# Kernel optimization log

Hardware: AMD Instinct MI355X
Metric: run time of the kernel (lower is better)

## Reference

```python
import jax, jax.numpy as jnp
import numpy as np


def make_dictionary(T, Drr, Dtheta):
    # rows i=0..T-1; (-Drr)**i == (-1)**i * Drr**i for integer i
    idx = jnp.arange(T, dtype=Drr.dtype)[:, None]                      # [T,1]
    sign = jnp.where(jnp.arange(T)[:, None] % 2 == 0, 1.0, -1.0).astype(Drr.dtype)
    ri = Drr[None, :] ** idx                                           # [T,N]
    c = jnp.cos(idx * Dtheta[None, :])
    s = jnp.sin(idx * Dtheta[None, :])
    dic = jnp.concatenate(
        [jnp.ones((T, 1), Drr.dtype), ri * c, sign * ri * c, ri * s, sign * ri * s],
        axis=1,
    )                                                                  # [T, 1+4N]
    G = jnp.linalg.norm(dic, axis=0)
    G = jnp.where(G == 0, jnp.sqrt(jnp.asarray(T, dic.dtype)), G)
    return dic / G


def softshrink(x, lam):
    return jnp.sign(x) * jnp.maximum(jnp.abs(x) - lam, 0.0)


def fista(D, Y, lambd=0.1, max_iter=100, tol=1e-4):
    # D: [T,K], Y: [B,T,F]
    K = D.shape[1]
    DtD = D.T @ D                                                      # [K,K]
    linv = 1.0 / jnp.linalg.norm(DtD)  # torch.norm(DtD, 2) == Frobenius norm
    DtY = jnp.einsum('tk,btf->bkf', D, Y) * linv                       # [B,K,F]
    A = jnp.eye(K, dtype=D.dtype) - DtD * linv
    lam = lambd * linv
    x0 = jnp.zeros_like(DtY)

    def cond(s):
        _, _, _, it, done = s
        return (it < max_iter) & jnp.logical_not(done)

    def body(s):
        x_old, y_old, t, it, done = s
        x_new = softshrink(jnp.einsum('kj,bjf->bkf', A, y_old) + DtY, lam)
        t_new = (1.0 + jnp.sqrt(1.0 + 4.0 * t * t)) / 2.0
        tt = (t - 1.0) / t_new
        y_new = (1.0 + tt) * x_new - tt * x_old
        conv = jnp.linalg.norm((x_new - x_old).ravel()) / K < tol
        return (x_new, y_new, jnp.where(conv, t, t_new), it + 1, conv)

    s0 = (x0, x0, jnp.asarray(1.0, D.dtype), jnp.asarray(0, jnp.int32),
          jnp.asarray(False))
    x, _, _, _, _ = jax.lax.while_loop(cond, body, s0)
    return x


def setup_inputs() -> dict:
    key = jax.random.key(0)
    k1, k2, k3 = jax.random.split(key, 3)
    return {
        'x': jax.random.normal(k1, (2, 36, 20480), jnp.float32),
        'Drr': jax.random.uniform(k2, (40,), dtype=jnp.float32),
        'Dtheta': jax.random.uniform(k3, (40,), dtype=jnp.float32),
        'T': 36,
    }


def reference(x, Drr, Dtheta, T):
    D = make_dictionary(T, Drr, Dtheta)
    return fista(D, x, lambd=0.1, max_iter=100)
```

## Files before the change

### kernel.cpp

```cpp
#include <hip/hip_runtime.h>
#include <math.h>

typedef _Float16 half8 __attribute__((ext_vector_type(8)));
typedef _Float16 half4 __attribute__((ext_vector_type(4)));
typedef float    f32x4 __attribute__((ext_vector_type(4)));

#define T_DIM 36
#define N_AT 40
#define K_REAL 161
#define MT 12
#define KS 6
#define KS2 2
#define B_DIM 2
#define F_DIM 20480
#define CB 16
#define MLOC 3
#define NTHREADS 256
#define SETUP_T 512
#define MAXIT 100
#define YK 200
#define YST 72

#define WS_AFRAG_OFF 64
#define AFRAG_BYTES (144 * 1024)
#define WS_DFRAG_OFF (WS_AFRAG_OFF + AFRAG_BYTES)

#define MFMA16(a, b, c) __builtin_amdgcn_mfma_f32_16x16x32_f16((a), (b), (c), 0, 0, 0)

__global__ void setup_kernel(const float* __restrict__ Drr,
                             const float* __restrict__ Dtheta,
                             float* __restrict__ ws) {
    __shared__ float Dl[K_REAL][T_DIM];
    __shared__ float red[SETUP_T];
    __shared__ float s_linv;
    int tid = threadIdx.x;

    if (tid < K_REAL) {
        float col[T_DIM];
        if (tid == 0) {
            for (int i = 0; i < T_DIM; ++i) col[i] = 1.0f;
        } else {
            int q = (tid - 1) / N_AT, n = (tid - 1) % N_AT;
            float r = Drr[n], th = Dtheta[n];
            float ri = 1.0f;
            for (int i = 0; i < T_DIM; ++i) {
                float c = cosf((float)i * th), s = sinf((float)i * th);
                float sign = (i & 1) ? -1.0f : 1.0f;
                float v;
                if (q == 0)      v = ri * c;
                else if (q == 1) v = sign * ri * c;
                else if (q == 2) v = ri * s;
                else             v = sign * ri * s;
                col[i] = v;
                ri *= r;
            }
        }
        float ss = 0.0f;
        for (int i = 0; i < T_DIM; ++i) ss += col[i] * col[i];
        float G = sqrtf(ss);
        float Ginv = (G == 0.0f) ? (1.0f / sqrtf((float)T_DIM)) : (1.0f / G);
        for (int i = 0; i < T_DIM; ++i) Dl[tid][i] = col[i] * Ginv;
    }
    __syncthreads();

    float local = 0.0f;
    for (int p = tid; p < K_REAL * K_REAL; p += SETUP_T) {
        int a = p / K_REAL, b = p % K_REAL;
        float dot = 0.0f;
        for (int i = 0; i < T_DIM; ++i) dot += Dl[a][i] * Dl[b][i];
        local += dot * dot;
    }
    red[tid] = local;
    __syncthreads();
    if (tid == 0) {
        float tot = 0.0f;
        for (int i = 0; i < SETUP_T; ++i) tot += red[i];
        float linv = 1.0f / sqrtf(tot);
        s_linv = linv;
        ws[0] = linv;
        ws[1] = 0.1f * linv;
    }
    __syncthreads();
    float linv = s_linv;

    _Float16* wsA = (_Float16*)((char*)ws + WS_AFRAG_OFF);
    int lane = tid >> 3, e = tid & 7;
    int fm = lane & 15, fq = lane >> 4;
    for (int p = 0; p < MT * KS; ++p) {
        int Mt = p / KS, ks = p % KS;
        int m = Mt * 16 + fm;
        int k = ks * 32 + fq * 8 + e;
        float v = 0.0f;
        if (m < K_REAL && k < K_REAL) {
            float dot = 0.0f;
            for (int t = 0; t < T_DIM; ++t) dot += Dl[m][t] * Dl[k][t];
            v = ((m == k) ? 1.0f : 0.0f) - linv * dot;
        }
        _Float16 h = (_Float16)v;
        _Float16 l = (_Float16)(v - (float)h);
        int base = (p * 2) * 512 + lane * 8 + e;
        wsA[base]       = h;
        wsA[base + 512] = l;
    }

    _Float16* wsD = (_Float16*)((char*)ws + WS_DFRAG_OFF);
    for (int p = 0; p < MT * KS2; ++p) {
        int Mt = p / KS2, ks2 = p % KS2;
        int kr = Mt * 16 + fm;
        int t  = ks2 * 32 + fq * 8 + e;
        float v = (kr < K_REAL && t < T_DIM) ? linv * Dl[kr][t] : 0.0f;
        _Float16 h = (_Float16)v;
        _Float16 l = (_Float16)(v - (float)h);
        int base = (p * 2) * 512 + lane * 8 + e;
        wsD[base]       = h;
        wsD[base + 512] = l;
    }
}

__global__ void __launch_bounds__(NTHREADS, 2)
fista_mfma(const float* __restrict__ Y, const float* __restrict__ ws,
           float* __restrict__ out) {
    __shared__ __align__(16) _Float16 ybuf[2][2][CB][YK];

    const float lam = ((const float*)ws)[1];
    const half8* Afp = (const half8*)((const char*)ws + WS_AFRAG_OFF);
    const half8* Dfp = (const half8*)((const char*)ws + WS_DFRAG_OFF);

    const int tid  = threadIdx.x;
    const int lane = tid & 63;
    const int mg   = __builtin_amdgcn_readfirstlane(tid >> 6);
    const int quad = lane >> 4;
    const int cl   = lane & 15;

    const int blk = blockIdx.x;
    const int b   = blk / (F_DIM / CB);
    const int f0  = (blk % (F_DIM / CB)) * CB;

    _Float16* Yst = &ybuf[1][0][0][0];
    const float* Yb = Y + (size_t)b * T_DIM * F_DIM + f0;
    for (int idx = tid; idx < 64 * CB; idx += NTHREADS) {
        int t = idx / CB, c = idx % CB;
        float v = (t < T_DIM) ? Yb[(size_t)t * F_DIM + c] : 0.0f;
        _Float16 h = (_Float16)v;
        _Float16 l = (_Float16)(v - (float)h);
        Yst[c * YST + t]            = h;
        Yst[CB * YST + c * YST + t] = l;
    }
    int4* zb = (int4*)&ybuf[0][0][0][0];
    for (int idx = tid; idx < (2 * CB * YK * 2) / 16; idx += NTHREADS)
        zb[idx] = int4{0, 0, 0, 0};
    __syncthreads();

    f32x4 dty[MLOC];
    #pragma unroll
    for (int ml = 0; ml < MLOC; ++ml) dty[ml] = f32x4{0.f, 0.f, 0.f, 0.f};
    #pragma unroll
    for (int ks2 = 0; ks2 < KS2; ++ks2) {
        const _Float16* yp = Yst + cl * YST + ks2 * 32 + quad * 8;
        half8 yh = *(const half8*)yp;
        half8 yl = *(const half8*)(yp + CB * YST);
        #pragma unroll
        for (int ml = 0; ml < MLOC; ++ml) {
            int Mt = mg * MLOC + ml;
            half8 dh = Dfp[((Mt * KS2 + ks2) * 2 + 0) * 64 + lane];
            half8 dl = Dfp[((Mt * KS2 + ks2) * 2 + 1) * 64 + lane];
            dty[ml] = MFMA16(dh, yh, dty[ml]);
            dty[ml] = MFMA16(dh, yl, dty[ml]);
            dty[ml] = MFMA16(dl, yh, dty[ml]);
        }
    }
    __syncthreads();

    half8 Af[MLOC][KS][2];
    #pragma unroll
    for (int ml = 0; ml < MLOC; ++ml)
        #pragma unroll
        for (int ks = 0; ks < KS; ++ks)
            #pragma unroll
            for (int term = 0; term < 2; ++term)
                Af[ml][ks][term] =
                    Afp[(((mg * MLOC + ml) * KS + ks) * 2 + term) * 64 + lane];

    float xold[MLOC][4];
    #pragma unroll
    for (int ml = 0; ml < MLOC; ++ml)
        #pragma unroll
        for (int r = 0; r < 4; ++r) xold[ml][r] = 0.0f;

    float tm = 1.0f;
    int p = 0;
    for (int it = 0; it < MAXIT; ++it) {
        f32x4 acc[MLOC];
        #pragma unroll
        for (int ml = 0; ml < MLOC; ++ml) acc[ml] = dty[ml];

        #pragma unroll
        for (int ks = 0; ks < KS; ++ks) {
            const _Float16* yp = &ybuf[p][0][cl][ks * 32 + quad * 8];
            half8 yh = *(const half8*)yp;
            half8 yl = *(const half8*)(yp + CB * YK);
            #pragma unroll
            for (int ml = 0; ml < MLOC; ++ml) {
                acc[ml] = MFMA16(Af[ml][ks][0], yh, acc[ml]);
                acc[ml] = MFMA16(Af[ml][ks][0], yl, acc[ml]);
                acc[ml] = MFMA16(Af[ml][ks][1], yh, acc[ml]);
            }
        }

        float tn = 0.5f * (1.0f + sqrtf(1.0f + 4.0f * tm * tm));
        float tt = (tm - 1.0f) / tn;
        tm = tn;

        #pragma unroll
        for (int ml = 0; ml < MLOC; ++ml) {
            half4 hv, lv;
            #pragma unroll
            for (int r = 0; r < 4; ++r) {
                float v  = acc[ml][r];
                float s  = fmaxf(fabsf(v) - lam, 0.0f);
                float xn = copysignf(s, v);
                float yn = (1.0f + tt) * xn - tt * xold[ml][r];
                xold[ml][r] = xn;
                _Float16 h = (_Float16)yn;
                hv[r] = h;
                lv[r] = (_Float16)(yn - (float)h);
            }
            int k0 = (mg * MLOC + ml) * 16 + quad * 4;
            *(half4*)&ybuf[1 - p][0][cl][k0] = hv;
            *(half4*)&ybuf[1 - p][1][cl][k0] = lv;
        }
        __syncthreads();
        p ^= 1;
    }

    float* ob = out + (size_t)b * K_REAL * F_DIM + f0 + cl;
    #pragma unroll
    for (int ml = 0; ml < MLOC; ++ml)
        #pragma unroll
        for (int r = 0; r < 4; ++r) {
            int k = (mg * MLOC + ml) * 16 + quad * 4 + r;
            if (k < K_REAL) ob[(size_t)k * F_DIM] = xold[ml][r];
        }
}

extern "C" void kernel_launch(void* const* d_in, const int* in_sizes, int n_in,
                              void* d_out, int out_size, void* d_ws, size_t ws_size,
                              hipStream_t stream) {
    const float* x      = (const float*)d_in[0];
    const float* Drr    = (const float*)d_in[1];
    const float* Dtheta = (const float*)d_in[2];
    float* out = (float*)d_out;
    float* ws  = (float*)d_ws;

    hipLaunchKernelGGL(setup_kernel, dim3(1), dim3(SETUP_T), 0, stream,
                       Drr, Dtheta, ws);
    hipLaunchKernelGGL(fista_mfma, dim3((B_DIM * F_DIM) / CB), dim3(NTHREADS),
                       0, stream, x, ws, out);
}
```

Measured before the change: 689.1 us.

## Switch FISTA iteration to 32x32x16 MFMA tiles with 32-column blocks

Replaces the 16x16x32 MFMA tiling with 32x32x16 MFMA. Each of six waves now owns a 32-row slice of the 192-padded coefficient dimension, and each block covers 32 F-columns instead of 16. The aim is to cut padding waste on the K dimension (from 192 to 176) and to halve the block count, so each A-fragment load and barrier serves more columns. The cost is larger per-wave accumulators and a changed occupancy target, and the last wave only partly fills its rows.

```diff
diff --git a/kernel.cpp b/kernel.cpp
--- a/kernel.cpp
+++ b/kernel.cpp
@@ -1,31 +1,32 @@
 #include <hip/hip_runtime.h>
 #include <math.h>
 
-typedef _Float16 half8 __attribute__((ext_vector_type(8)));
-typedef _Float16 half4 __attribute__((ext_vector_type(4)));
-typedef float    f32x4 __attribute__((ext_vector_type(4)));
+typedef _Float16 half8  __attribute__((ext_vector_type(8)));
+typedef _Float16 half4  __attribute__((ext_vector_type(4)));
+typedef float    f32x16 __attribute__((ext_vector_type(16)));
 
 #define T_DIM 36
 #define N_AT 40
 #define K_REAL 161
-#define MT 12
-#define KS 6
-#define KS2 2
+#define MT32 6
+#define KS16 11
+#define KT 3
 #define B_DIM 2
 #define F_DIM 20480
-#define CB 16
-#define MLOC 3
-#define NTHREADS 256
+#define CB 32
+#define NW 6
+#define NTHREADS (NW * 64)
 #define SETUP_T 512
 #define MAXIT 100
-#define YK 200
-#define YST 72
+#define YKH 200
+#define YSTH 104
 
 #define WS_AFRAG_OFF 64
-#define AFRAG_BYTES (144 * 1024)
+#define AFRAG_BYTES (MT32 * KS16 * 2 * 1024)
 #define WS_DFRAG_OFF (WS_AFRAG_OFF + AFRAG_BYTES)
-
-#define MFMA16(a, b, c) __builtin_amdgcn_mfma_f32_16x16x32_f16((a), (b), (c), 0, 0, 0)
+#define DFRAG_BYTES (MT32 * KT * 2 * 1024)
+
+#define MFMA32(a, b, c) __builtin_amdgcn_mfma_f32_32x32x16_f16((a), (b), (c), 0, 0, 0)
 
 __global__ void setup_kernel(const float* __restrict__ Drr,
                              const float* __restrict__ Dtheta,
@@ -85,11 +86,11 @@
 
     _Float16* wsA = (_Float16*)((char*)ws + WS_AFRAG_OFF);
     int lane = tid >> 3, e = tid & 7;
-    int fm = lane & 15, fq = lane >> 4;
-    for (int p = 0; p < MT * KS; ++p) {
-        int Mt = p / KS, ks = p % KS;
-        int m = Mt * 16 + fm;
-        int k = ks * 32 + fq * 8 + e;
+    int fm = lane & 31, fg = lane >> 5;
+    for (int p = 0; p < MT32 * KS16; ++p) {
+        int Mt = p / KS16, ks = p % KS16;
+        int m = Mt * 32 + fm;
+        int k = ks * 16 + fg * 8 + e;
         float v = 0.0f;
         if (m < K_REAL && k < K_REAL) {
             float dot = 0.0f;
@@ -104,10 +105,10 @@
     }
 
     _Float16* wsD = (_Float16*)((char*)ws + WS_DFRAG_OFF);
-    for (int p = 0; p < MT * KS2; ++p) {
-        int Mt = p / KS2, ks2 = p % KS2;
-        int kr = Mt * 16 + fm;
-        int t  = ks2 * 32 + fq * 8 + e;
+    for (int p = 0; p < MT32 * KT; ++p) {
+        int Mt = p / KT, ks2 = p % KT;
+        int kr = Mt * 32 + fm;
+        int t  = ks2 * 16 + fg * 8 + e;
         float v = (kr < K_REAL && t < T_DIM) ? linv * Dl[kr][t] : 0.0f;
         _Float16 h = (_Float16)v;
         _Float16 l = (_Float16)(v - (float)h);
@@ -117,10 +118,10 @@
     }
 }
 
-__global__ void __launch_bounds__(NTHREADS, 2)
+__global__ void __launch_bounds__(NTHREADS, 3)
 fista_mfma(const float* __restrict__ Y, const float* __restrict__ ws,
            float* __restrict__ out) {
-    __shared__ __align__(16) _Float16 ybuf[2][2][CB][YK];
+    __shared__ __align__(16) _Float16 ybuf[2][2][CB][YKH];
 
     const float lam = ((const float*)ws)[1];
     const half8* Afp = (const half8*)((const char*)ws + WS_AFRAG_OFF);
@@ -129,8 +130,8 @@
     const int tid  = threadIdx.x;
     const int lane = tid & 63;
     const int mg   = __builtin_amdgcn_readfirstlane(tid >> 6);
-    const int quad = lane >> 4;
-    const int cl   = lane & 15;
+    const int col  = lane & 31;
+    const int kg   = lane >> 5;
 
     const int blk = blockIdx.x;
     const int b   = blk / (F_DIM / CB);
@@ -138,73 +139,59 @@
 
     _Float16* Yst = &ybuf[1][0][0][0];
     const float* Yb = Y + (size_t)b * T_DIM * F_DIM + f0;
-    for (int idx = tid; idx < 64 * CB; idx += NTHREADS) {
-        int t = idx / CB, c = idx % CB;
+    for (int idx = tid; idx < 48 * CB; idx += NTHREADS) {
+        int t = idx >> 5, c = idx & 31;
         float v = (t < T_DIM) ? Yb[(size_t)t * F_DIM + c] : 0.0f;
         _Float16 h = (_Float16)v;
         _Float16 l = (_Float16)(v - (float)h);
-        Yst[c * YST + t]            = h;
-        Yst[CB * YST + c * YST + t] = l;
+        Yst[c * YSTH + t]             = h;
+        Yst[CB * YSTH + c * YSTH + t] = l;
     }
     int4* zb = (int4*)&ybuf[0][0][0][0];
-    for (int idx = tid; idx < (2 * CB * YK * 2) / 16; idx += NTHREADS)
+    for (int idx = tid; idx < (2 * CB * YKH * 2) / 16; idx += NTHREADS)
         zb[idx] = int4{0, 0, 0, 0};
     __syncthreads();
 
-    f32x4 dty[MLOC];
-    #pragma unroll
-    for (int ml = 0; ml < MLOC; ++ml) dty[ml] = f32x4{0.f, 0.f, 0.f, 0.f};
-    #pragma unroll
-    for (int ks2 = 0; ks2 < KS2; ++ks2) {
-        const _Float16* yp = Yst + cl * YST + ks2 * 32 + quad * 8;
+    f32x16 dty;
+    #pragma unroll
+    for (int r = 0; r < 16; ++r) dty[r] = 0.0f;
+    #pragma unroll
+    for (int ks2 = 0; ks2 < KT; ++ks2) {
+        const _Float16* yp = Yst + col * YSTH + ks2 * 16 + kg * 8;
         half8 yh = *(const half8*)yp;
-        half8 yl = *(const half8*)(yp + CB * YST);
+        half8 yl = *(const half8*)(yp + CB * YSTH);
+        half8 dh = Dfp[((mg * KT + ks2) * 2 + 0) * 64 + lane];
+        half8 dl = Dfp[((mg * KT + ks2) * 2 + 1) * 64 + lane];
+        dty = MFMA32(dh, yh, dty);
+        dty = MFMA32(dh, yl, dty);
+        dty = MFMA32(dl, yh, dty);
+    }
+    __syncthreads();
+
+    half8 Af[KS16][2];
+    #pragma unroll
+    for (int ks = 0; ks < KS16; ++ks)
         #pragma unroll
-        for (int ml = 0; ml < MLOC; ++ml) {
-            int Mt = mg * MLOC + ml;
-            half8 dh = Dfp[((Mt * KS2 + ks2) * 2 + 0) * 64 + lane];
-            half8 dl = Dfp[((Mt * KS2 + ks2) * 2 + 1) * 64 + lane];
-            dty[ml] = MFMA16(dh, yh, dty[ml]);
-            dty[ml] = MFMA16(dh, yl, dty[ml]);
-            dty[ml] = MFMA16(dl, yh, dty[ml]);
-        }
-    }
-    __syncthreads();
-
-    half8 Af[MLOC][KS][2];
-    #pragma unroll
-    for (int ml = 0; ml < MLOC; ++ml)
-        #pragma unroll
-        for (int ks = 0; ks < KS; ++ks)
-            #pragma unroll
-            for (int term = 0; term < 2; ++term)
-                Af[ml][ks][term] =
-                    Afp[(((mg * MLOC + ml) * KS + ks) * 2 + term) * 64 + lane];
-
-    float xold[MLOC][4];
-    #pragma unroll
-    for (int ml = 0; ml < MLOC; ++ml)
-        #pragma unroll
-        for (int r = 0; r < 4; ++r) xold[ml][r] = 0.0f;
+        for (int term = 0; term < 2; ++term)
+            Af[ks][term] = Afp[((mg * KS16 + ks) * 2 + term) * 64 + lane];
+
+    float xold[16];
+    #pragma unroll
+    for (int r = 0; r < 16; ++r) xold[r] = 0.0f;
 
     float tm = 1.0f;
     int p = 0;
     for (int it = 0; it < MAXIT; ++it) {
-        f32x4 acc[MLOC];
+        f32x16 acc = dty;
+
         #pragma unroll
-        for (int ml = 0; ml < MLOC; ++ml) acc[ml] = dty[ml];
-
-        #pragma unroll
-        for (int ks = 0; ks < KS; ++ks) {
-            const _Float16* yp = &ybuf[p][0][cl][ks * 32 + quad * 8];
+        for (int ks = 0; ks < KS16; ++ks) {
+            const _Float16* yp = &ybuf[p][0][col][ks * 16 + kg * 8];
             half8 yh = *(const half8*)yp;
-            half8 yl = *(const half8*)(yp + CB * YK);
-            #pragma unroll
-            for (int ml = 0; ml < MLOC; ++ml) {
-                acc[ml] = MFMA16(Af[ml][ks][0], yh, acc[ml]);
-                acc[ml] = MFMA16(Af[ml][ks][0], yl, acc[ml]);
-                acc[ml] = MFMA16(Af[ml][ks][1], yh, acc[ml]);
-            }
+            half8 yl = *(const half8*)(yp + CB * YKH);
+            acc = MFMA32(Af[ks][0], yh, acc);
+            acc = MFMA32(Af[ks][0], yl, acc);
+            acc = MFMA32(Af[ks][1], yh, acc);
         }
 
         float tn = 0.5f * (1.0f + sqrtf(1.0f + 4.0f * tm * tm));
@@ -212,35 +199,36 @@
         tm = tn;
 
         #pragma unroll
-        for (int ml = 0; ml < MLOC; ++ml) {
-            half4 hv, lv;
-            #pragma unroll
-            for (int r = 0; r < 4; ++r) {
-                float v  = acc[ml][r];
-                float s  = fmaxf(fabsf(v) - lam, 0.0f);
-                float xn = copysignf(s, v);
-                float yn = (1.0f + tt) * xn - tt * xold[ml][r];
-                xold[ml][r] = xn;
-                _Float16 h = (_Float16)yn;
-                hv[r] = h;
-                lv[r] = (_Float16)(yn - (float)h);
+        for (int c4 = 0; c4 < 4; ++c4) {
+            if (mg < 5 || c4 < 2) {
+                half4 hv, lv;
+                #pragma unroll
+                for (int j = 0; j < 4; ++j) {
+                    int r = c4 * 4 + j;
+                    float v  = acc[r];
+                    float s  = fmaxf(fabsf(v) - lam, 0.0f);
+                    float xn = copysignf(s, v);
+                    float yn = (1.0f + tt) * xn - tt * xold[r];
+                    xold[r] = xn;
+                    _Float16 h = (_Float16)yn;
+                    hv[j] = h;
+                    lv[j] = (_Float16)(yn - (float)h);
+                }
+                int kh = mg * 32 + c4 * 8 + kg * 4;
+                *(half4*)&ybuf[1 - p][0][col][kh] = hv;
+                *(half4*)&ybuf[1 - p][1][col][kh] = lv;
             }
-            int k0 = (mg * MLOC + ml) * 16 + quad * 4;
-            *(half4*)&ybuf[1 - p][0][cl][k0] = hv;
-            *(half4*)&ybuf[1 - p][1][cl][k0] = lv;
         }
         __syncthreads();
         p ^= 1;
     }
 
-    float* ob = out + (size_t)b * K_REAL * F_DIM + f0 + cl;
-    #pragma unroll
-    for (int ml = 0; ml < MLOC; ++ml)
-        #pragma unroll
-        for (int r = 0; r < 4; ++r) {
-            int k = (mg * MLOC + ml) * 16 + quad * 4 + r;
-            if (k < K_REAL) ob[(size_t)k * F_DIM] = xold[ml][r];
-        }
+    float* ob = out + (size_t)b * K_REAL * F_DIM + f0 + col;
+    #pragma unroll
+    for (int r = 0; r < 16; ++r) {
+        int k = mg * 32 + (r >> 2) * 8 + kg * 4 + (r & 3);
+        if (k < K_REAL) ob[(size_t)k * F_DIM] = xold[r];
+    }
 }
 
 extern "C" void kernel_launch(void* const* d_in, const int* in_sizes, int n_in,
```

Result: slower. 837.0 us (+21.5%).
